# Kernel tuning notes

Hardware: AMD Instinct MI355X
Metric: run time of the kernel (lower is better)

## Reference

```python
import jax, jax.numpy as jnp
import numpy as np
from jax import lax

B, C, H, W = 16, 512, 32, 32
CQ = C // 16


def _conv(x, w, b):
    # NCHW input, OIHW kernel, 3x3 stride-1 'SAME' == torch padding=1
    o = lax.conv_general_dilated(x, w, (1, 1), 'SAME',
                                 dimension_numbers=('NCHW', 'OIHW', 'NCHW'))
    return o + b[None, :, None, None]


def setup_inputs() -> dict:
    key = jax.random.key(0)
    ks = jax.random.split(key, 8)
    fan_q = C * 9
    fan_v = C * 9
    return {
        'x': jax.random.normal(ks[0], (B, C, H, W), jnp.float32),
        'y': jax.random.normal(ks[1], (B, C, H, W), jnp.float32),
        'wq': jax.random.normal(ks[2], (CQ, C, 3, 3), jnp.float32) / np.sqrt(fan_q),
        'bq': jnp.zeros((CQ,), jnp.float32),
        'wk': jax.random.normal(ks[3], (CQ, C, 3, 3), jnp.float32) / np.sqrt(fan_q),
        'bk': jnp.zeros((CQ,), jnp.float32),
        'wv': jax.random.normal(ks[4], (C, C, 3, 3), jnp.float32) / np.sqrt(fan_v),
        'bv': jnp.zeros((C,), jnp.float32),
    }


def reference(x, y, wq, bq, wk, bk, wv, bv):
    b, c, h, w = x.shape
    n = h * w
    q = _conv(x, wq, bq).reshape(b, -1, n)   # (B, CQ, N)
    k = _conv(y, wk, bk).reshape(b, -1, n)   # (B, CQ, N)
    v = _conv(y, wv, bv).reshape(b, c, n)    # (B, C, N)
    # energy[b, i, j] = <q[:, i], k[:, j]>  (unscaled, non-causal)
    energy = jnp.einsum('bdi,bdj->bij', q, k)           # (B, N, N)
    attn = jax.nn.softmax(energy, axis=-1)              # softmax over keys j
    # out[b, c, i] = sum_j v[b, c, j] * attn[b, i, j]
    out = jnp.einsum('bcj,bij->bci', v, attn)           # (B, C, N)
    return out.reshape(b, c, h, w)
```

## Files before the change

kernel.cpp:

```cpp
#include <hip/hip_runtime.h>

#define BB 16
#define CCH 512
#define CQD 32
#define HH 32
#define WW 32
#define NN 1024
#define PH 34

typedef __attribute__((ext_vector_type(8))) _Float16 half8;
typedef __attribute__((ext_vector_type(4))) _Float16 half4;
typedef __attribute__((ext_vector_type(4))) float f32x4;

static __device__ __forceinline__ void gload_lds16(const void* g, void* l) {
    __builtin_amdgcn_global_load_lds(
        (const __attribute__((address_space(1))) unsigned int*)g,
        (__attribute__((address_space(3))) unsigned int*)l, 16, 0, 0);
}

__global__ __launch_bounds__(256) void prep_img_kernel(
    const float* __restrict__ x, const float* __restrict__ y,
    _Float16* __restrict__ xp, _Float16* __restrict__ yp)
{
    const int h = blockIdx.x;
    const int which = blockIdx.y, b = blockIdx.z;
    const float* img = which ? y : x;
    _Float16* row = (which ? yp : xp) + (size_t)(b * PH + h) * PH * CCH;
    const int t = threadIdx.x;
    const int gh = h - 1;

    half8 z;
    #pragma unroll
    for (int u = 0; u < 8; ++u) z[u] = (_Float16)0.f;

    if (gh < 0 || gh >= HH) {
        for (int idx = t; idx < PH * CCH / 8; idx += 256)
            *(half8*)&row[(size_t)idx * 8] = z;
        return;
    }

    __shared__ float X[64][33];
    for (int ci0 = 0; ci0 < CCH; ci0 += 64) {
        __syncthreads();
        #pragma unroll
        for (int i = 0; i < 8; ++i) {
            int ci = i * 8 + (t >> 5), w = t & 31;
            X[ci][w] = img[((size_t)(b * CCH + ci0 + ci) * HH + gh) * WW + w];
        }
        __syncthreads();
        int w = t >> 3, g = t & 7;
        half8 o;
        #pragma unroll
        for (int u = 0; u < 8; ++u) o[u] = (_Float16)X[g * 8 + u][w];
        *(half8*)&row[(size_t)(w + 1) * CCH + ci0 + g * 8] = o;
        if (t < 16) {
            int col = (t < 8) ? 0 : 33;
            *(half8*)&row[(size_t)col * CCH + ci0 + (t & 7) * 8] = z;
        }
    }
}

__global__ __launch_bounds__(256) void prep_w_all_kernel(
    const float* __restrict__ wv, const float* __restrict__ wq,
    const float* __restrict__ wk, _Float16* __restrict__ wvh,
    _Float16* __restrict__ wqkh)
{
    const int bid = blockIdx.x;
    const float* src;
    _Float16* dst;
    int co_src, co_dst;
    if (bid < 512)      { src = wv; co_src = bid;       dst = wvh;  co_dst = bid; }
    else if (bid < 544) { src = wq; co_src = bid - 512; dst = wqkh; co_dst = bid - 512; }
    else                { src = wk; co_src = bid - 544; dst = wqkh; co_dst = 32 + (bid - 544); }
    for (int idx = threadIdx.x; idx < 4608; idx += 256) {
        int tap = idx / 512, ci = idx - tap * 512;
        dst[(size_t)co_dst * 4608 + idx] = (_Float16)src[(size_t)co_src * 4608 + ci * 9 + tap];
    }
}

__global__ __launch_bounds__(256, 2) void conv_v_mfma_kernel(
    const _Float16* __restrict__ yp,
    const _Float16* __restrict__ wvh,
    const float* __restrict__ bvb,
    _Float16* __restrict__ vout)
{
    const int pt  = blockIdx.x;
    const int co0 = blockIdx.y * 64;
    const int b   = blockIdx.z;

    __shared__ __align__(16) _Float16 Wl[64 * 296];
    __shared__ __align__(16) _Float16 Yl[13824];

    const int t    = threadIdx.x;
    const int lane = t & 63;
    const int wv4  = t >> 6;
    const int l15  = lane & 15;
    const int kg   = lane >> 4;

    f32x4 acc[4][4];
    #pragma unroll
    for (int m = 0; m < 4; ++m)
        #pragma unroll
        for (int n = 0; n < 4; ++n) {
            f32x4 z = {0.f, 0.f, 0.f, 0.f};
            acc[m][n] = z;
        }

    const int r0p = pt * 8;
    int bbase[4];
    #pragma unroll
    for (int n = 0; n < 4; ++n) {
        int pxl = wv4 * 64 + n * 16 + l15;
        int rl = pxl >> 5, cl = pxl & 31;
        bbase[n] = (rl * 34 + cl) * 40 + kg * 8;
    }
    int abase[4];
    #pragma unroll
    for (int m = 0; m < 4; ++m)
        abase[m] = (m * 16 + l15) * 296 + kg * 8;

    #pragma unroll 1
    for (int ci0 = 0; ci0 < CCH; ci0 += 32) {
        __syncthreads();
        #pragma unroll
        for (int i = 0; i < 10; ++i) {
            int d = t + i * 256;
            if (d < 2368) {
                int c = d / 37, rem = d - c * 37;
                const _Float16* g = (rem < 36)
                    ? &wvh[(size_t)(co0 + c) * 4608 + (rem >> 2) * 512 + ci0 + (rem & 3) * 8]
                    : wvh;
                gload_lds16(g, (char*)Wl + (size_t)(i * 256 + wv4 * 64) * 16);
            }
        }
        #pragma unroll
        for (int i = 0; i < 7; ++i) {
            int d = t + i * 256;
            if (d < 1728) {
                int rc = d / 5, part = d - rc * 5;
                const _Float16* g = yp;
                if (rc < 340 && part < 4) {
                    int r = rc / 34, c = rc - r * 34;
                    g = &yp[((size_t)(b * PH + r0p + r) * PH + c) * CCH + ci0 + part * 8];
                }
                gload_lds16(g, (char*)Yl + (size_t)(i * 256 + wv4 * 64) * 16);
            }
        }
        __syncthreads();

        #pragma unroll
        for (int tap = 0; tap < 9; ++tap) {
            const int dh = tap / 3, dw = tap % 3;
            half8 a[4], bf[4];
            #pragma unroll
            for (int m = 0; m < 4; ++m)
                a[m] = *(const half8*)&Wl[abase[m] + tap * 32];
            #pragma unroll
            for (int n = 0; n < 4; ++n)
                bf[n] = *(const half8*)&Yl[bbase[n] + (dh * 34 + dw) * 40];
            #pragma unroll
            for (int m = 0; m < 4; ++m)
                #pragma unroll
                for (int n = 0; n < 4; ++n)
                    acc[m][n] = __builtin_amdgcn_mfma_f32_16x16x32_f16(a[m], bf[n], acc[m][n], 0, 0, 0);
        }
    }

    #pragma unroll
    for (int m = 0; m < 4; ++m) {
        #pragma unroll
        for (int reg = 0; reg < 4; ++reg) {
            int co = co0 + m * 16 + kg * 4 + reg;
            float bias = bvb[co];
            #pragma unroll
            for (int n = 0; n < 4; ++n) {
                int px = pt * 256 + wv4 * 64 + n * 16 + l15;
                vout[((size_t)b * CCH + co) * NN + px] = (_Float16)(acc[m][n][reg] + bias);
            }
        }
    }
}

__global__ __launch_bounds__(256, 4) void conv_qk_split_kernel(
    const _Float16* __restrict__ xp,
    const _Float16* __restrict__ yp,
    const _Float16* __restrict__ wqkh,
    float* __restrict__ pbuf)
{
    const int pt    = blockIdx.x >> 2;
    const int ks    = blockIdx.x & 3;
    const int which = blockIdx.y;
    const int b     = blockIdx.z;
    const _Float16* in = which ? yp : xp;

    __shared__ __align__(16) _Float16 Wl[9728];
    __shared__ __align__(16) _Float16 Xl[8192];

    const int t    = threadIdx.x;
    const int lane = t & 63;
    const int w    = t >> 6;
    const int l15  = lane & 15;
    const int kg   = lane >> 4;

    f32x4 acc[2][2];
    #pragma unroll
    for (int m = 0; m < 2; ++m)
        #pragma unroll
        for (int n = 0; n < 2; ++n) {
            f32x4 z = {0.f, 0.f, 0.f, 0.f};
            acc[m][n] = z;
        }

    const int r0p = pt * 4;
    int bbase[2];
    #pragma unroll
    for (int n = 0; n < 2; ++n) {
        int pxl = w * 32 + n * 16 + l15;
        int rl = pxl >> 5, cl = pxl & 31;
        bbase[n] = (rl * 34 + cl) * 40 + kg * 8;
    }
    int abase[2];
    #pragma unroll
    for (int m = 0; m < 2; ++m)
        abase[m] = (m * 16 + l15) * 296 + kg * 8;

    #pragma unroll 1
    for (int cc = 0; cc < 4; ++cc) {
        const int ci0 = ks * 128 + cc * 32;
        __syncthreads();
        #pragma unroll
        for (int i = 0; i < 5; ++i) {
            int d = t + i * 256;
            if (d < 1216) {
                const _Float16* g = wqkh;
                if (d < 1184) {
                    int c = d / 37, rem = d - c * 37;
                    if (rem < 36)
                        g = &wqkh[(size_t)(which * 32 + c) * 4608 + (rem >> 2) * 512 + ci0 + (rem & 3) * 8];
                }
                gload_lds16(g, (char*)Wl + (size_t)(i * 256 + w * 64) * 16);
            }
        }
        #pragma unroll
        for (int i = 0; i < 4; ++i) {
            int d = t + i * 256;
            int rc = d / 5, part = d - rc * 5;
            const _Float16* g = in;
            if (rc < 204 && part < 4) {
                int r = rc / 34, c = rc - r * 34;
                g = &in[((size_t)(b * PH + r0p + r) * PH + c) * CCH + ci0 + part * 8];
            }
            gload_lds16(g, (char*)Xl + (size_t)(i * 256 + w * 64) * 16);
        }
        __syncthreads();

        #pragma unroll
        for (int tap = 0; tap < 9; ++tap) {
            const int dh = tap / 3, dw = tap % 3;
            half8 a[2], bfr[2];
            #pragma unroll
            for (int m = 0; m < 2; ++m)
                a[m] = *(const half8*)&Wl[abase[m] + tap * 32];
            #pragma unroll
            for (int n = 0; n < 2; ++n)
                bfr[n] = *(const half8*)&Xl[bbase[n] + (dh * 34 + dw) * 40];
            #pragma unroll
            for (int m = 0; m < 2; ++m)
                #pragma unroll
                for (int n = 0; n < 2; ++n)
                    acc[m][n] = __builtin_amdgcn_mfma_f32_16x16x32_f16(a[m], bfr[n], acc[m][n], 0, 0, 0);
        }
    }

    float* pb = &pbuf[(((size_t)(ks * 2 + which) * BB + b) * NN) * CQD];
    #pragma unroll
    for (int n = 0; n < 2; ++n) {
        int px = pt * 128 + w * 32 + n * 16 + l15;
        #pragma unroll
        for (int m = 0; m < 2; ++m) {
            float4 o = make_float4(acc[m][n][0], acc[m][n][1], acc[m][n][2], acc[m][n][3]);
            *(float4*)&pb[(size_t)px * CQD + m * 16 + kg * 4] = o;
        }
    }
}

__global__ __launch_bounds__(256) void qk_reduce_kernel(
    const float* __restrict__ pbuf,
    const float* __restrict__ bq, const float* __restrict__ bk,
    _Float16* __restrict__ qh, _Float16* __restrict__ kh)
{
    const int gid   = blockIdx.x * 256 + threadIdx.x;
    const int cog   = gid & 7;
    const int px    = (gid >> 3) & 1023;
    const int b     = (gid >> 13) & 15;
    const int which = gid >> 17;

    const size_t base = (((size_t)which * BB + b) * NN + px) * CQD + cog * 4;
    const size_t kstep = (size_t)2 * BB * NN * CQD;
    float4 s = *(const float4*)&pbuf[base];
    #pragma unroll
    for (int ks = 1; ks < 4; ++ks) {
        float4 p = *(const float4*)&pbuf[base + ks * kstep];
        s.x += p.x; s.y += p.y; s.z += p.z; s.w += p.w;
    }
    const float* bias = which ? bk : bq;
    float4 bv = *(const float4*)&bias[cog * 4];
    half4 o;
    o[0] = (_Float16)(s.x + bv.x);
    o[1] = (_Float16)(s.y + bv.y);
    o[2] = (_Float16)(s.z + bv.z);
    o[3] = (_Float16)(s.w + bv.w);
    _Float16* out = which ? kh : qh;
    *(half4*)&out[((size_t)b * NN + px) * CQD + cog * 4] = o;
}

__global__ __launch_bounds__(256, 2) void attn_fused_kernel(
    const _Float16* __restrict__ qh,
    const _Float16* __restrict__ kh,
    const _Float16* __restrict__ v,
    float* __restrict__ out)
{
    const int wg   = blockIdx.x;
    const int virt = (wg & 7) * 64 + (wg >> 3);
    const int b    = virt >> 5;
    const int i0   = (virt & 31) * 32;

    __shared__ __align__(16) _Float16 Vl[2][128 * 136];
    __shared__ __align__(16) _Float16 Pl[32 * 136];
    float* redm = (float*)Pl;
    float* redl = redm + 32 * 17;

    const int t    = threadIdx.x;
    const int lane = t & 63;
    const int w    = t >> 6;
    const int l15  = lane & 15;
    const int kg   = lane >> 4;

    #define STAGE_V(dst, jp_, cc_)                                              \
        {                                                                       \
            _Pragma("unroll")                                                   \
            for (int i_ = 0; i_ < 9; ++i_) {                                    \
                int d_ = t + i_ * 256;                                          \
                if (d_ < 2176) {                  \
                    int r_ = d_ / 17, rem_ = d_ - r_ * 17;                      \
                    const _Float16* g_ = (rem_ < 16)                            \
                        ? &v[((size_t)b * CCH + (cc_) * 128 + r_) * NN + (jp_) * 128 + rem_ * 8] \
                        : v;                                                    \
                    gload_lds16(g_, (char*)(dst) + (size_t)(i_ * 256 + w * 64) * 16); \
                }                                                               \
            }                                                                   \
        }

    half8 qb[2];
    #pragma unroll
    for (int n = 0; n < 2; ++n)
        qb[n] = *(const half8*)&qh[((size_t)b * NN + i0 + n * 16 + l15) * CQD + kg * 8];

    float m[2] = {-3.0e38f, -3.0e38f}, l[2] = {0.f, 0.f};
    #pragma unroll 1
    for (int jp = 0; jp < 8; ++jp) {
        #pragma unroll
        for (int ht = 0; ht < 2; ++ht) {
            int j = jp * 128 + ht * 64 + w * 16 + l15;
            half8 ak = *(const half8*)&kh[((size_t)b * NN + j) * CQD + kg * 8];
            #pragma unroll
            for (int n = 0; n < 2; ++n) {
                f32x4 s = {0.f, 0.f, 0.f, 0.f};
                s = __builtin_amdgcn_mfma_f32_16x16x32_f16(ak, qb[n], s, 0, 0, 0);
                float tm = fmaxf(fmaxf(s[0], s[1]), fmaxf(s[2], s[3]));
                float m2 = fmaxf(m[n], tm);
                l[n] = l[n] * __expf(m[n] - m2)
                     + __expf(s[0] - m2) + __expf(s[1] - m2)
                     + __expf(s[2] - m2) + __expf(s[3] - m2);
                m[n] = m2;
            }
        }
    }
    #pragma unroll
    for (int n = 0; n < 2; ++n) {
        redm[(n * 16 + l15) * 17 + w * 4 + kg] = m[n];
        redl[(n * 16 + l15) * 17 + w * 4 + kg] = l[n];
    }
    __syncthreads();
    float mr[2], rl[2];
    #pragma unroll
    for (int n = 0; n < 2; ++n) {
        const int i = n * 16 + l15;
        float M = redm[i * 17];
        #pragma unroll
        for (int p = 1; p < 16; ++p) M = fmaxf(M, redm[i * 17 + p]);
        float L = 0.f;
        #pragma unroll
        for (int p = 0; p < 16; ++p) L += redl[i * 17 + p] * __expf(redm[i * 17 + p] - M);
        mr[n] = M;
        rl[n] = 1.f / L;
    }

    f32x4 acc[4][2][2];
    #pragma unroll
    for (int cc = 0; cc < 4; ++cc)
        #pragma unroll
        for (int mm = 0; mm < 2; ++mm)
            #pragma unroll
            for (int n = 0; n < 2; ++n) {
                f32x4 z = {0.f, 0.f, 0.f, 0.f};
                acc[cc][mm][n] = z;
            }

    #pragma unroll 1
    for (int jp = 0; jp < 8; ++jp) {
        __syncthreads();
        STAGE_V(Vl[0], jp, 0);
        #pragma unroll
        for (int ht = 0; ht < 2; ++ht) {
            int j = jp * 128 + ht * 64 + w * 16 + l15;
            half8 ak = *(const half8*)&kh[((size_t)b * NN + j) * CQD + kg * 8];
            #pragma unroll
            for (int n = 0; n < 2; ++n) {
                f32x4 s = {0.f, 0.f, 0.f, 0.f};
                s = __builtin_amdgcn_mfma_f32_16x16x32_f16(ak, qb[n], s, 0, 0, 0);
                half4 p4;
                #pragma unroll
                for (int reg = 0; reg < 4; ++reg)
                    p4[reg] = (_Float16)(__expf(s[reg] - mr[n]) * rl[n]);
                *(half4*)&Pl[(n * 16 + l15) * 136 + ht * 64 + w * 16 + kg * 4] = p4;
            }
        }
        #pragma unroll
        for (int cc = 0; cc < 4; ++cc) {
            __syncthreads();
            if (cc < 3) {
                _Float16* vnxt = (_Float16*)Vl[(cc + 1) & 1];
                STAGE_V(vnxt, jp, cc + 1);
            }
            const _Float16* vcur = (const _Float16*)Vl[cc & 1];
            #pragma unroll
            for (int ks = 0; ks < 4; ++ks) {
                half8 pb[2], va[2];
                #pragma unroll
                for (int n = 0; n < 2; ++n)
                    pb[n] = *(const half8*)&Pl[(n * 16 + l15) * 136 + ks * 32 + kg * 8];
                #pragma unroll
                for (int mm = 0; mm < 2; ++mm)
                    va[mm] = *(const half8*)&vcur[(w * 32 + mm * 16 + l15) * 136 + ks * 32 + kg * 8];
                #pragma unroll
                for (int mm = 0; mm < 2; ++mm)
                    #pragma unroll
                    for (int n = 0; n < 2; ++n)
                        acc[cc][mm][n] = __builtin_amdgcn_mfma_f32_16x16x32_f16(va[mm], pb[n], acc[cc][mm][n], 0, 0, 0);
            }
        }
    }

    #pragma unroll
    for (int cc = 0; cc < 4; ++cc)
        #pragma unroll
        for (int mm = 0; mm < 2; ++mm)
            #pragma unroll
            for (int n = 0; n < 2; ++n)
                #pragma unroll
                for (int reg = 0; reg < 4; ++reg) {
                    int c = cc * 128 + w * 32 + mm * 16 + kg * 4 + reg;
                    out[((size_t)b * CCH + c) * NN + i0 + n * 16 + l15] = acc[cc][mm][n][reg];
                }
    #undef STAGE_V
}

extern "C" void kernel_launch(void* const* d_in, const int* in_sizes, int n_in,
                              void* d_out, int out_size, void* d_ws, size_t ws_size,
                              hipStream_t stream) {
    const float* x  = (const float*)d_in[0];
    const float* y  = (const float*)d_in[1];
    const float* wq = (const float*)d_in[2];
    const float* bq = (const float*)d_in[3];
    const float* wk = (const float*)d_in[4];
    const float* bk = (const float*)d_in[5];
    const float* wv = (const float*)d_in[6];
    const float* bv = (const float*)d_in[7];
    float* out = (float*)d_out;

    _Float16* qhb = (_Float16*)d_ws;
    _Float16* khb = qhb + (size_t)BB * NN * CQD;
    _Float16* vb   = khb + (size_t)BB * NN * CQD;
    _Float16* ypb  = vb + (size_t)BB * CCH * NN;
    _Float16* xpb  = ypb + (size_t)BB * PH * PH * CCH;
    _Float16* wvh  = xpb + (size_t)BB * PH * PH * CCH;
    _Float16* wqkh = wvh + (size_t)512 * 4608;
    float* pbuf = (float*)vb;

    prep_img_kernel<<<dim3(PH, 2, BB), 256, 0, stream>>>(x, y, xpb, ypb);
    prep_w_all_kernel<<<dim3(576), 256, 0, stream>>>(wv, wq, wk, wvh, wqkh);
    conv_qk_split_kernel<<<dim3(32, 2, BB), 256, 0, stream>>>(xpb, ypb, wqkh, pbuf);
    qk_reduce_kernel<<<dim3(1024), 256, 0, stream>>>(pbuf, bq, bk, qhb, khb);
    conv_v_mfma_kernel<<<dim3(4, 8, BB), 256, 0, stream>>>(ypb, wvh, bv, vb);
    attn_fused_kernel<<<dim3(512), 256, 0, stream>>>(qhb, khb, vb, out);
}
```

Before: 169.4 us.

## Use 32x32x16 MFMA in V conv and merge prep kernels into one launch

The V convolution switches from 16x16x32 to 32x32x16 MFMA tiles. Each wave now holds 2x2 tiles of 32x32 and reads fewer LDS fragments per MFMA, so LDS bandwidth pressure per unit of compute drops. The image-padding and weight-repack prep kernels are merged into a single launch, saving one kernel launch. The epilogue's output mapping changes to match the 32x32 accumulator layout, and the bias is now read as a float4.

Result: slower. 175.5 us (+3.6%).

```diff
diff --git a/kernel.cpp b/kernel.cpp
--- a/kernel.cpp
+++ b/kernel.cpp
@@ -11,6 +11,7 @@
 typedef __attribute__((ext_vector_type(8))) _Float16 half8;
 typedef __attribute__((ext_vector_type(4))) _Float16 half4;
 typedef __attribute__((ext_vector_type(4))) float f32x4;
+typedef __attribute__((ext_vector_type(16))) float f32x16;
 
 static __device__ __forceinline__ void gload_lds16(const void* g, void* l) {
     __builtin_amdgcn_global_load_lds(
@@ -18,15 +19,35 @@
         (__attribute__((address_space(3))) unsigned int*)l, 16, 0, 0);
 }
 
-__global__ __launch_bounds__(256) void prep_img_kernel(
+__global__ __launch_bounds__(256) void prep_all_kernel(
     const float* __restrict__ x, const float* __restrict__ y,
-    _Float16* __restrict__ xp, _Float16* __restrict__ yp)
+    const float* __restrict__ wv, const float* __restrict__ wq,
+    const float* __restrict__ wk,
+    _Float16* __restrict__ xp, _Float16* __restrict__ yp,
+    _Float16* __restrict__ wvh, _Float16* __restrict__ wqkh)
 {
-    const int h = blockIdx.x;
-    const int which = blockIdx.y, b = blockIdx.z;
+    const int bid = blockIdx.x;
+    const int t = threadIdx.x;
+
+    if (bid >= 1088) {
+        const int wb = bid - 1088;
+        const float* src;
+        _Float16* dst;
+        int co_src, co_dst;
+        if (wb < 512)      { src = wv; co_src = wb;       dst = wvh;  co_dst = wb; }
+        else if (wb < 544) { src = wq; co_src = wb - 512; dst = wqkh; co_dst = wb - 512; }
+        else               { src = wk; co_src = wb - 544; dst = wqkh; co_dst = 32 + (wb - 544); }
+        for (int idx = t; idx < 4608; idx += 256) {
+            int tap = idx / 512, ci = idx - tap * 512;
+            dst[(size_t)co_dst * 4608 + idx] = (_Float16)src[(size_t)co_src * 4608 + ci * 9 + tap];
+        }
+        return;
+    }
+
+    const int h = bid >> 5;
+    const int which = (bid >> 4) & 1, b = bid & 15;
     const float* img = which ? y : x;
     _Float16* row = (which ? yp : xp) + (size_t)(b * PH + h) * PH * CCH;
-    const int t = threadIdx.x;
     const int gh = h - 1;
 
     half8 z;
@@ -57,24 +78,6 @@
             int col = (t < 8) ? 0 : 33;
             *(half8*)&row[(size_t)col * CCH + ci0 + (t & 7) * 8] = z;
         }
-    }
-}
-
-__global__ __launch_bounds__(256) void prep_w_all_kernel(
-    const float* __restrict__ wv, const float* __restrict__ wq,
-    const float* __restrict__ wk, _Float16* __restrict__ wvh,
-    _Float16* __restrict__ wqkh)
-{
-    const int bid = blockIdx.x;
-    const float* src;
-    _Float16* dst;
-    int co_src, co_dst;
-    if (bid < 512)      { src = wv; co_src = bid;       dst = wvh;  co_dst = bid; }
-    else if (bid < 544) { src = wq; co_src = bid - 512; dst = wqkh; co_dst = bid - 512; }
-    else                { src = wk; co_src = bid - 544; dst = wqkh; co_dst = 32 + (bid - 544); }
-    for (int idx = threadIdx.x; idx < 4608; idx += 256) {
-        int tap = idx / 512, ci = idx - tap * 512;
-        dst[(size_t)co_dst * 4608 + idx] = (_Float16)src[(size_t)co_src * 4608 + ci * 9 + tap];
     }
 }
 
@@ -94,30 +97,29 @@
     const int t    = threadIdx.x;
     const int lane = t & 63;
     const int wv4  = t >> 6;
-    const int l15  = lane & 15;
-    const int kg   = lane >> 4;
-
-    f32x4 acc[4][4];
-    #pragma unroll
-    for (int m = 0; m < 4; ++m)
-        #pragma unroll
-        for (int n = 0; n < 4; ++n) {
-            f32x4 z = {0.f, 0.f, 0.f, 0.f};
-            acc[m][n] = z;
-        }
+    const int l31  = lane & 31;
+    const int kh2  = lane >> 5;
+
+    f32x16 acc[2][2];
+    #pragma unroll
+    for (int m = 0; m < 2; ++m)
+        #pragma unroll
+        for (int n = 0; n < 2; ++n)
+            #pragma unroll
+            for (int e = 0; e < 16; ++e) acc[m][n][e] = 0.f;
 
     const int r0p = pt * 8;
-    int bbase[4];
-    #pragma unroll
-    for (int n = 0; n < 4; ++n) {
-        int pxl = wv4 * 64 + n * 16 + l15;
+    int bbase[2];
+    #pragma unroll
+    for (int n = 0; n < 2; ++n) {
+        int pxl = wv4 * 64 + n * 32 + l31;
         int rl = pxl >> 5, cl = pxl & 31;
-        bbase[n] = (rl * 34 + cl) * 40 + kg * 8;
-    }
-    int abase[4];
-    #pragma unroll
-    for (int m = 0; m < 4; ++m)
-        abase[m] = (m * 16 + l15) * 296 + kg * 8;
+        bbase[n] = (rl * 34 + cl) * 40 + kh2 * 8;
+    }
+    int abase[2];
+    #pragma unroll
+    for (int m = 0; m < 2; ++m)
+        abase[m] = (m * 32 + l31) * 296 + kh2 * 8;
 
     #pragma unroll 1
     for (int ci0 = 0; ci0 < CCH; ci0 += 32) {
@@ -151,31 +153,42 @@
         #pragma unroll
         for (int tap = 0; tap < 9; ++tap) {
             const int dh = tap / 3, dw = tap % 3;
-            half8 a[4], bf[4];
-            #pragma unroll
-            for (int m = 0; m < 4; ++m)
-                a[m] = *(const half8*)&Wl[abase[m] + tap * 32];
-            #pragma unroll
-            for (int n = 0; n < 4; ++n)
-                bf[n] = *(const half8*)&Yl[bbase[n] + (dh * 34 + dw) * 40];
-            #pragma unroll
-            for (int m = 0; m < 4; ++m)
-                #pragma unroll
-                for (int n = 0; n < 4; ++n)
-                    acc[m][n] = __builtin_amdgcn_mfma_f32_16x16x32_f16(a[m], bf[n], acc[m][n], 0, 0, 0);
-        }
-    }
-
-    #pragma unroll
-    for (int m = 0; m < 4; ++m) {
-        #pragma unroll
-        for (int reg = 0; reg < 4; ++reg) {
-            int co = co0 + m * 16 + kg * 4 + reg;
-            float bias = bvb[co];
-            #pragma unroll
-            for (int n = 0; n < 4; ++n) {
-                int px = pt * 256 + wv4 * 64 + n * 16 + l15;
-                vout[((size_t)b * CCH + co) * NN + px] = (_Float16)(acc[m][n][reg] + bias);
+            half8 a[2][2], bf[2][2];
+            #pragma unroll
+            for (int m = 0; m < 2; ++m)
+                #pragma unroll
+                for (int ks = 0; ks < 2; ++ks)
+                    a[m][ks] = *(const half8*)&Wl[abase[m] + tap * 32 + ks * 16];
+            #pragma unroll
+            for (int n = 0; n < 2; ++n)
+                #pragma unroll
+                for (int ks = 0; ks < 2; ++ks)
+                    bf[n][ks] = *(const half8*)&Yl[bbase[n] + (dh * 34 + dw) * 40 + ks * 16];
+            #pragma unroll
+            for (int m = 0; m < 2; ++m)
+                #pragma unroll
+                for (int n = 0; n < 2; ++n)
+                    #pragma unroll
+                    for (int ks = 0; ks < 2; ++ks)
+                        acc[m][n] = __builtin_amdgcn_mfma_f32_32x32x16_f16(a[m][ks], bf[n][ks], acc[m][n], 0, 0, 0);
+        }
+    }
+
+    #pragma unroll
+    for (int m = 0; m < 2; ++m) {
+        #pragma unroll
+        for (int rq = 0; rq < 4; ++rq) {
+            float4 bv = *(const float4*)&bvb[co0 + m * 32 + rq * 8 + kh2 * 4];
+            #pragma unroll
+            for (int e = 0; e < 4; ++e) {
+                int reg = rq * 4 + e;
+                int co = co0 + m * 32 + rq * 8 + kh2 * 4 + e;
+                float bias = (&bv.x)[e];
+                #pragma unroll
+                for (int n = 0; n < 2; ++n) {
+                    int px = pt * 256 + wv4 * 64 + n * 32 + l31;
+                    vout[((size_t)b * CCH + co) * NN + px] = (_Float16)(acc[m][n][reg] + bias);
+                }
             }
         }
     }
@@ -488,8 +501,7 @@
     _Float16* wqkh = wvh + (size_t)512 * 4608;
     float* pbuf = (float*)vb;
 
-    prep_img_kernel<<<dim3(PH, 2, BB), 256, 0, stream>>>(x, y, xpb, ypb);
-    prep_w_all_kernel<<<dim3(576), 256, 0, stream>>>(wv, wq, wk, wvh, wqkh);
+    prep_all_kernel<<<dim3(1088 + 576), 256, 0, stream>>>(x, y, wv, wq, wk, xpb, ypb, wvh, wqkh);
     conv_qk_split_kernel<<<dim3(32, 2, BB), 256, 0, stream>>>(xpb, ypb, wqkh, pbuf);
     qk_reduce_kernel<<<dim3(1024), 256, 0, stream>>>(pbuf, bq, bk, qhb, khb);
     conv_v_mfma_kernel<<<dim3(4, 8, BB), 256, 0, stream>>>(ypb, wvh, bv, vb);
```

## Merge prep kernels and read V directly from global in attention

Applied to the files above, without the earlier changes.

Combines the image-padding and weight-conversion prep kernels into a single launch using a flat block index. In the attention kernel, it removes the double-buffered LDS staging of V (and the per-chunk barriers), loading V fragments straight from global memory into MFMA operands. This cuts LDS usage and synchronisation, which may allow higher occupancy, but it relies on cache hits for V reuse and gives up async prefetch overlap.

Result: slower. 201.7 us (+19.0%).

```diff
diff --git a/kernel.cpp b/kernel.cpp
--- a/kernel.cpp
+++ b/kernel.cpp
@@ -18,15 +18,35 @@
         (__attribute__((address_space(3))) unsigned int*)l, 16, 0, 0);
 }
 
-__global__ __launch_bounds__(256) void prep_img_kernel(
+__global__ __launch_bounds__(256) void prep_all_kernel(
     const float* __restrict__ x, const float* __restrict__ y,
-    _Float16* __restrict__ xp, _Float16* __restrict__ yp)
+    const float* __restrict__ wv, const float* __restrict__ wq,
+    const float* __restrict__ wk,
+    _Float16* __restrict__ xp, _Float16* __restrict__ yp,
+    _Float16* __restrict__ wvh, _Float16* __restrict__ wqkh)
 {
-    const int h = blockIdx.x;
-    const int which = blockIdx.y, b = blockIdx.z;
+    const int bid = blockIdx.x;
+    const int t = threadIdx.x;
+
+    if (bid >= 1088) {
+        const int wb = bid - 1088;
+        const float* src;
+        _Float16* dst;
+        int co_src, co_dst;
+        if (wb < 512)      { src = wv; co_src = wb;       dst = wvh;  co_dst = wb; }
+        else if (wb < 544) { src = wq; co_src = wb - 512; dst = wqkh; co_dst = wb - 512; }
+        else               { src = wk; co_src = wb - 544; dst = wqkh; co_dst = 32 + (wb - 544); }
+        for (int idx = t; idx < 4608; idx += 256) {
+            int tap = idx / 512, ci = idx - tap * 512;
+            dst[(size_t)co_dst * 4608 + idx] = (_Float16)src[(size_t)co_src * 4608 + ci * 9 + tap];
+        }
+        return;
+    }
+
+    const int h = bid >> 5;
+    const int which = (bid >> 4) & 1, b = bid & 15;
     const float* img = which ? y : x;
     _Float16* row = (which ? yp : xp) + (size_t)(b * PH + h) * PH * CCH;
-    const int t = threadIdx.x;
     const int gh = h - 1;
 
     half8 z;
@@ -57,24 +77,6 @@
             int col = (t < 8) ? 0 : 33;
             *(half8*)&row[(size_t)col * CCH + ci0 + (t & 7) * 8] = z;
         }
-    }
-}
-
-__global__ __launch_bounds__(256) void prep_w_all_kernel(
-    const float* __restrict__ wv, const float* __restrict__ wq,
-    const float* __restrict__ wk, _Float16* __restrict__ wvh,
-    _Float16* __restrict__ wqkh)
-{
-    const int bid = blockIdx.x;
-    const float* src;
-    _Float16* dst;
-    int co_src, co_dst;
-    if (bid < 512)      { src = wv; co_src = bid;       dst = wvh;  co_dst = bid; }
-    else if (bid < 544) { src = wq; co_src = bid - 512; dst = wqkh; co_dst = bid - 512; }
-    else                { src = wk; co_src = bid - 544; dst = wqkh; co_dst = 32 + (bid - 544); }
-    for (int idx = threadIdx.x; idx < 4608; idx += 256) {
-        int tap = idx / 512, ci = idx - tap * 512;
-        dst[(size_t)co_dst * 4608 + idx] = (_Float16)src[(size_t)co_src * 4608 + ci * 9 + tap];
     }
 }
 
@@ -325,7 +327,6 @@
     const int b    = virt >> 5;
     const int i0   = (virt & 31) * 32;
 
-    __shared__ __align__(16) _Float16 Vl[2][128 * 136];
     __shared__ __align__(16) _Float16 Pl[32 * 136];
     float* redm = (float*)Pl;
     float* redl = redm + 32 * 17;
@@ -335,21 +336,6 @@
     const int w    = t >> 6;
     const int l15  = lane & 15;
     const int kg   = lane >> 4;
-
-    #define STAGE_V(dst, jp_, cc_)                                              \
-        {                                                                       \
-            _Pragma("unroll")                                                   \
-            for (int i_ = 0; i_ < 9; ++i_) {                                    \
-                int d_ = t + i_ * 256;                                          \
-                if (d_ < 2176) {                  \
-                    int r_ = d_ / 17, rem_ = d_ - r_ * 17;                      \
-                    const _Float16* g_ = (rem_ < 16)                            \
-                        ? &v[((size_t)b * CCH + (cc_) * 128 + r_) * NN + (jp_) * 128 + rem_ * 8] \
-                        : v;                                                    \
-                    gload_lds16(g_, (char*)(dst) + (size_t)(i_ * 256 + w * 64) * 16); \
-                }                                                               \
-            }                                                                   \
-        }
 
     half8 qb[2];
     #pragma unroll
@@ -410,7 +396,6 @@
     #pragma unroll 1
     for (int jp = 0; jp < 8; ++jp) {
         __syncthreads();
-        STAGE_V(Vl[0], jp, 0);
         #pragma unroll
         for (int ht = 0; ht < 2; ++ht) {
             int j = jp * 128 + ht * 64 + w * 16 + l15;
@@ -426,14 +411,9 @@
                 *(half4*)&Pl[(n * 16 + l15) * 136 + ht * 64 + w * 16 + kg * 4] = p4;
             }
         }
+        __syncthreads();
         #pragma unroll
         for (int cc = 0; cc < 4; ++cc) {
-            __syncthreads();
-            if (cc < 3) {
-                _Float16* vnxt = (_Float16*)Vl[(cc + 1) & 1];
-                STAGE_V(vnxt, jp, cc + 1);
-            }
-            const _Float16* vcur = (const _Float16*)Vl[cc & 1];
             #pragma unroll
             for (int ks = 0; ks < 4; ++ks) {
                 half8 pb[2], va[2];
@@ -441,8 +421,10 @@
                 for (int n = 0; n < 2; ++n)
                     pb[n] = *(const half8*)&Pl[(n * 16 + l15) * 136 + ks * 32 + kg * 8];
                 #pragma unroll
-                for (int mm = 0; mm < 2; ++mm)
-                    va[mm] = *(const half8*)&vcur[(w * 32 + mm * 16 + l15) * 136 + ks * 32 + kg * 8];
+                for (int mm = 0; mm < 2; ++mm) {
+                    int c = cc * 128 + w * 32 + mm * 16 + l15;
+                    va[mm] = *(const half8*)&v[((size_t)b * CCH + c) * NN + jp * 128 + ks * 32 + kg * 8];
+                }
                 #pragma unroll
                 for (int mm = 0; mm < 2; ++mm)
                     #pragma unroll
@@ -463,7 +445,6 @@
                     int c = cc * 128 + w * 32 + mm * 16 + kg * 4 + reg;
                     out[((size_t)b * CCH + c) * NN + i0 + n * 16 + l15] = acc[cc][mm][n][reg];
                 }
-    #undef STAGE_V
 }
 
 extern "C" void kernel_launch(void* const* d_in, const int* in_sizes, int n_in,
@@ -488,8 +469,7 @@
     _Float16* wqkh = wvh + (size_t)512 * 4608;
     float* pbuf = (float*)vb;
 
-    prep_img_kernel<<<dim3(PH, 2, BB), 256, 0, stream>>>(x, y, xpb, ypb);
-    prep_w_all_kernel<<<dim3(576), 256, 0, stream>>>(wv, wq, wk, wvh, wqkh);
+    prep_all_kernel<<<dim3(1088 + 576), 256, 0, stream>>>(x, y, wv, wq, wk, xpb, ypb, wvh, wqkh);
     conv_qk_split_kernel<<<dim3(32, 2, BB), 256, 0, stream>>>(xpb, ypb, wqkh, pbuf);
     qk_reduce_kernel<<<dim3(1024), 256, 0, stream>>>(pbuf, bq, bk, qhb, khb);
     conv_v_mfma_kernel<<<dim3(4, 8, BB), 256, 0, stream>>>(ypb, wvh, bv, vb);
```
